# Kernel optimization log

Hardware: AMD Instinct MI355X
Metric: run time of the kernel (lower is better)

Reference implementation:

```python
import jax, jax.numpy as jnp
import numpy as np

B, S, H, D = 1, 2048, 16, 128
HID = H * D  # 2048
EPS = 1e-6


def setup_inputs() -> dict:
    key = jax.random.key(0)
    ks = jax.random.split(key, 6)
    sc = 1.0 / np.sqrt(HID)
    t = jnp.arange(S, dtype=jnp.float32)[:, None]
    inv = 1.0 / (10000.0 ** (jnp.arange(D // 2, dtype=jnp.float32) / (D // 2)))
    ang = t * inv[None, :]
    return {
        "hidden_states": jax.random.normal(ks[0], (B, S, HID), jnp.float32),
        "freqs_cos": jnp.cos(ang),
        "freqs_sin": jnp.sin(ang),
        "w_qkv": jax.random.normal(ks[1], (HID, 3 * HID), jnp.float32) * sc,
        "b_qkv": jnp.zeros((3 * HID,), jnp.float32),
        "w_norm_q": jnp.ones((HID,), jnp.float32),
        "w_norm_k": jnp.ones((HID,), jnp.float32),
        "w_out": jax.random.normal(ks[2], (HID, HID), jnp.float32) * sc,
        "b_out": jnp.zeros((HID,), jnp.float32),
    }


def _rmsnorm(x, w):
    var = jnp.mean(jnp.square(x), axis=-1, keepdims=True)
    return x * jax.lax.rsqrt(var + EPS) * w


def _rope(x, cos, sin):
    # x: [B, H, S, D]; cos/sin: [S, D//2], interleaved pair rotation
    xr = x.reshape(*x.shape[:-1], D // 2, 2)
    x1, x2 = xr[..., 0], xr[..., 1]
    c = cos[None, None, :, :]
    s = sin[None, None, :, :]
    o1 = x1 * c - x2 * s
    o2 = x1 * s + x2 * c
    return jnp.stack([o1, o2], axis=-1).reshape(x.shape)


def reference(hidden_states, freqs_cos, freqs_sin, w_qkv, b_qkv,
              w_norm_q, w_norm_k, w_out, b_out):
    qkv = hidden_states @ w_qkv + b_qkv  # [B, S, 3*HID]
    q, k, v = jnp.split(qkv, 3, axis=-1)
    q = _rmsnorm(q, w_norm_q).reshape(B, S, H, D).transpose(0, 2, 1, 3)
    k = _rmsnorm(k, w_norm_k).reshape(B, S, H, D).transpose(0, 2, 1, 3)
    v = v.reshape(B, S, H, D).transpose(0, 2, 1, 3)
    q = _rope(q, freqs_cos, freqs_sin)
    k = _rope(k, freqs_cos, freqs_sin)
    scale = 1.0 / np.sqrt(D)
    scores = jnp.einsum("bhqd,bhkd->bhqk", q, k) * scale
    attn = jax.nn.softmax(scores, axis=-1)
    out = jnp.einsum("bhqk,bhkd->bhqd", attn, v)
    out = out.transpose(0, 2, 1, 3).reshape(B, S, HID)
    return out @ w_out + b_out
```

## Files before the change

kernel.cpp:

```cpp
#include <hip/hip_runtime.h>
#include <math.h>

typedef unsigned short u16;
typedef __bf16 bf16x8 __attribute__((ext_vector_type(8)));
typedef float f32x4 __attribute__((ext_vector_type(4)));
typedef unsigned short u16x8 __attribute__((ext_vector_type(8)));

#define SLEN 2048
#define HIDN 2048
#define NH   16
#define DHD  128

static __device__ __forceinline__ float bf2f(u16 u) {
  unsigned int i = ((unsigned int)u) << 16;
  return __builtin_bit_cast(float, i);
}
static __device__ __forceinline__ u16 f2bf(float f) {
  unsigned int x = __builtin_bit_cast(unsigned int, f);
  unsigned int r = x + 0x7fffu + ((x >> 16) & 1u);
  return (u16)(r >> 16);
}
static __device__ __forceinline__ void gload_lds16(const u16* g, u16* l) {
  __builtin_amdgcn_global_load_lds((const __attribute__((address_space(1))) void*)g,
                                   (__attribute__((address_space(3))) void*)l,
                                   16, 0, 0);
}

__global__ __launch_bounds__(256) void transpcvt(const float* __restrict__ in,
                                                 u16* __restrict__ out,
                                                 int istride, int ostride) {
  __shared__ float tl[64][65];
  const int t = threadIdx.x;
  const int r0 = blockIdx.x * 64, c0 = blockIdx.y * 64;
#pragma unroll
  for (int it = 0; it < 4; ++it) {
    int row = it * 16 + (t >> 4);
    int col = (t & 15) * 4;
    f32x4 v = *(const f32x4*)&in[(size_t)(r0 + row) * istride + c0 + col];
    tl[row][col] = v[0]; tl[row][col + 1] = v[1];
    tl[row][col + 2] = v[2]; tl[row][col + 3] = v[3];
  }
  __syncthreads();
#pragma unroll
  for (int it = 0; it < 2; ++it) {
    int orow = it * 32 + (t >> 3);
    int ocol = (t & 7) * 8;
    u16x8 v;
#pragma unroll
    for (int j = 0; j < 8; ++j) v[j] = f2bf(tl[ocol + j][orow]);
    *(u16x8*)&out[(size_t)(c0 + orow) * ostride + r0 + ocol] = v;
  }
}

__global__ __launch_bounds__(256) void cvt_bf16(const float* __restrict__ in,
                                                u16* __restrict__ out) {
  int i = (blockIdx.x * 256 + threadIdx.x) * 8;
  f32x4 a = *(const f32x4*)&in[i];
  f32x4 b = *(const f32x4*)&in[i + 4];
  u16x8 v;
#pragma unroll
  for (int j = 0; j < 4; ++j) { v[j] = f2bf(a[j]); v[4 + j] = f2bf(b[j]); }
  *(u16x8*)&out[i] = v;
}

__global__ __launch_bounds__(256) void transp(const u16* __restrict__ in,
                                              u16* __restrict__ out,
                                              int istride, int ostride,
                                              int in_z, int out_z) {
  in  += (size_t)blockIdx.z * in_z;
  out += (size_t)blockIdx.z * out_z;
  __shared__ u16 tl[64][72];
  const int t  = threadIdx.x;
  const int r0 = blockIdx.x * 64, c0 = blockIdx.y * 64;
#pragma unroll
  for (int it = 0; it < 2; ++it) {
    int row = it * 32 + (t >> 3);
    int col = (t & 7) * 8;
    *(u16x8*)&tl[row][col] =
        *(const u16x8*)&in[(size_t)(r0 + row) * istride + c0 + col];
  }
  __syncthreads();
#pragma unroll
  for (int it = 0; it < 2; ++it) {
    int orow = it * 32 + (t >> 3);
    int ocol = (t & 7) * 8;
    u16x8 v;
#pragma unroll
    for (int j = 0; j < 8; ++j) v[j] = tl[ocol + j][orow];
    *(u16x8*)&out[(size_t)(c0 + orow) * ostride + r0 + ocol] = v;
  }
}

__global__ __launch_bounds__(256) void gemm_bt(const u16* __restrict__ A,
                                               const u16* __restrict__ BT,
                                               const float* __restrict__ bias,
                                               float* Cf, u16* Cb,
                                               int M, int N, int K) {
  __shared__ u16 lA[128 * 64];
  __shared__ u16 lB[128 * 64];
  const int t = threadIdx.x;
  const int lane = t & 63, w = t >> 6;
  const int g = lane >> 4, l16 = lane & 15;
  const int wr = w >> 1, wc = w & 1;
  const u16* Ab = A + (size_t)blockIdx.x * 128 * K;
  const u16* Bb = BT + (size_t)blockIdx.y * 128 * K;

  f32x4 acc[4][4];
#pragma unroll
  for (int mi = 0; mi < 4; ++mi)
#pragma unroll
    for (int ni = 0; ni < 4; ++ni) acc[mi][ni] = (f32x4)(0.0f);

  for (int k0 = 0; k0 < K; k0 += 64) {
    __syncthreads();
#pragma unroll
    for (int i = 0; i < 4; ++i) {
      int e = t * 8 + i * 2048;
      int row = e >> 6;
      int col16 = (e & 63) >> 3;
      int scol = (col16 ^ (row & 7)) * 8;
      gload_lds16(Ab + (size_t)row * K + k0 + scol, &lA[e]);
      gload_lds16(Bb + (size_t)row * K + k0 + scol, &lB[e]);
    }
    __syncthreads();
#pragma unroll
    for (int kk = 0; kk < 2; ++kk) {
      bf16x8 af[4], bfr[4];
#pragma unroll
      for (int mi = 0; mi < 4; ++mi) {
        int row = wr * 64 + mi * 16 + l16;
        af[mi] = *(const bf16x8*)&lA[row * 64 + (((4 * kk + g) ^ (l16 & 7)) << 3)];
      }
#pragma unroll
      for (int ni = 0; ni < 4; ++ni) {
        int row = wc * 64 + ni * 16 + l16;
        bfr[ni] = *(const bf16x8*)&lB[row * 64 + (((4 * kk + g) ^ (l16 & 7)) << 3)];
      }
#pragma unroll
      for (int mi = 0; mi < 4; ++mi)
#pragma unroll
        for (int ni = 0; ni < 4; ++ni)
          acc[mi][ni] = __builtin_amdgcn_mfma_f32_16x16x32_bf16(af[mi], bfr[ni],
                                                                acc[mi][ni], 0, 0, 0);
    }
  }

#pragma unroll
  for (int ni = 0; ni < 4; ++ni) {
    int n = blockIdx.y * 128 + wc * 64 + ni * 16 + l16;
    float bv = bias[n];
#pragma unroll
    for (int mi = 0; mi < 4; ++mi) {
      int m = blockIdx.x * 128 + wr * 64 + mi * 16 + 4 * g;
#pragma unroll
      for (int r = 0; r < 4; ++r) {
        float v = acc[mi][ni][r] + bv;
        if (Cf) Cf[(size_t)(m + r) * N + n] = v;
        else    Cb[(size_t)(m + r) * N + n] = f2bf(v);
      }
    }
  }
}

__global__ __launch_bounds__(256) void rms_rope(const u16* __restrict__ qkv,
                                                const float* __restrict__ fcos,
                                                const float* __restrict__ fsin,
                                                const float* __restrict__ wq,
                                                const float* __restrict__ wk,
                                                u16* __restrict__ Qr,
                                                u16* __restrict__ Kr) {
  const int s = blockIdx.x;
  const int t = threadIdx.x;
  const int lane = t & 63, w = t >> 6;
  __shared__ float red[2][4];
  const u16* row = qkv + (size_t)s * (3 * HIDN);

  u16x8 xq = *(const u16x8*)&row[t * 8];
  u16x8 xk = *(const u16x8*)&row[HIDN + t * 8];
  float fq[8], fk[8];
  float ssq = 0.f, ssk = 0.f;
#pragma unroll
  for (int j = 0; j < 8; ++j) {
    fq[j] = bf2f(xq[j]); ssq += fq[j] * fq[j];
    fk[j] = bf2f(xk[j]); ssk += fk[j] * fk[j];
  }
#pragma unroll
  for (int off = 32; off >= 1; off >>= 1) {
    ssq += __shfl_xor(ssq, off);
    ssk += __shfl_xor(ssk, off);
  }
  if (lane == 0) { red[0][w] = ssq; red[1][w] = ssk; }
  __syncthreads();
  float sq = red[0][0] + red[0][1] + red[0][2] + red[0][3];
  float sk = red[1][0] + red[1][1] + red[1][2] + red[1][3];
  float rq = rsqrtf(sq / (float)HIDN + 1e-6f);
  float rk = rsqrtf(sk / (float)HIDN + 1e-6f);

  f32x4 wq0 = *(const f32x4*)&wq[t * 8];
  f32x4 wq1 = *(const f32x4*)&wq[t * 8 + 4];
  f32x4 wk0 = *(const f32x4*)&wk[t * 8];
  f32x4 wk1 = *(const f32x4*)&wk[t * 8 + 4];
  float wqa[8] = {wq0[0], wq0[1], wq0[2], wq0[3], wq1[0], wq1[1], wq1[2], wq1[3]};
  float wka[8] = {wk0[0], wk0[1], wk0[2], wk0[3], wk1[0], wk1[1], wk1[2], wk1[3]};
  const int c0 = t * 8;
  const int h = c0 >> 7;
  const int d0 = c0 & 127;
  const int i0 = d0 >> 1;
  const float* cp = fcos + (size_t)s * (DHD / 2) + i0;
  const float* sp = fsin + (size_t)s * (DHD / 2) + i0;
  const float qscale = 0.12751744925f;

  u16x8 oq, ok;
#pragma unroll
  for (int p = 0; p < 4; ++p) {
    float c = cp[p], sn = sp[p];
    float q1 = fq[2 * p] * rq * wqa[2 * p];
    float q2 = fq[2 * p + 1] * rq * wqa[2 * p + 1];
    float k1 = fk[2 * p] * rk * wka[2 * p];
    float k2 = fk[2 * p + 1] * rk * wka[2 * p + 1];
    oq[2 * p]     = f2bf((q1 * c - q2 * sn) * qscale);
    oq[2 * p + 1] = f2bf((q1 * sn + q2 * c) * qscale);
    ok[2 * p]     = f2bf(k1 * c - k2 * sn);
    ok[2 * p + 1] = f2bf(k1 * sn + k2 * c);
  }
  size_t o = (size_t)h * SLEN * DHD + (size_t)s * DHD + d0;
  *(u16x8*)&Qr[o] = oq;
  *(u16x8*)&Kr[o] = ok;
}

__global__ __launch_bounds__(256) void attn_fwd(const u16* __restrict__ Qr,
                                                const u16* __restrict__ Kr,
                                                const u16* __restrict__ Vt,
                                                u16* __restrict__ out) {
  const int lin = blockIdx.x;
  const int xcd = lin & 7, idx = lin >> 3;
  const int h = xcd + ((idx >> 5) << 3);
  const int qb = idx & 31;
  const int t = threadIdx.x;
  const int lane = t & 63, w = t >> 6;
  const int g = lane >> 4, l16 = lane & 15;
  const int q0 = qb * 64 + w * 16;
  const u16* Qh = Qr + (size_t)h * SLEN * DHD;
  const u16* Kh = Kr + (size_t)h * SLEN * DHD;
  const u16* Vh = Vt + (size_t)h * DHD * SLEN;

  __shared__ u16 Kl[2][64 * 128];
  __shared__ u16 Vl[2][128 * 64];
  __shared__ u16 Pl[4][16][72];

  bf16x8 aq[4];
#pragma unroll
  for (int dk = 0; dk < 4; ++dk)
    aq[dk] = *(const bf16x8*)&Qh[(size_t)(q0 + l16) * DHD + dk * 32 + g * 8];

  f32x4 o[8];
#pragma unroll
  for (int df = 0; df < 8; ++df) o[df] = (f32x4)(0.0f);
  float m = -INFINITY, lsum = 0.f;

#pragma unroll
  for (int i = 0; i < 4; ++i) {
    int e = t * 8 + i * 2048;
    int kr = e >> 7, kc = (e & 127) >> 3;
    gload_lds16(Kh + (size_t)kr * DHD + ((kc ^ (kr & 7)) << 3), &Kl[0][e]);
    int vr = e >> 6, vc = (e & 63) >> 3;
    gload_lds16(Vh + (size_t)vr * SLEN + ((vc ^ (vr & 7)) << 3), &Vl[0][e]);
  }
  __syncthreads();

  int cur = 0;
  for (int kt = 0; kt < SLEN / 64; ++kt) {
    if (kt + 1 < SLEN / 64) {
      const int kv1 = (kt + 1) * 64;
#pragma unroll
      for (int i = 0; i < 4; ++i) {
        int e = t * 8 + i * 2048;
        int kr = e >> 7, kc = (e & 127) >> 3;
        gload_lds16(Kh + (size_t)(kv1 + kr) * DHD + ((kc ^ (kr & 7)) << 3),
                    &Kl[cur ^ 1][e]);
        int vr = e >> 6, vc = (e & 63) >> 3;
        gload_lds16(Vh + (size_t)vr * SLEN + kv1 + ((vc ^ (vr & 7)) << 3),
                    &Vl[cur ^ 1][e]);
      }
    }

    f32x4 s4[4];
#pragma unroll
    for (int nf = 0; nf < 4; ++nf) s4[nf] = (f32x4)(0.0f);
#pragma unroll
    for (int nf = 0; nf < 4; ++nf) {
#pragma unroll
      for (int dk = 0; dk < 4; ++dk) {
        bf16x8 bk = *(const bf16x8*)&Kl[cur][(nf * 16 + l16) * 128 +
                                            (((dk * 4 + g) ^ (l16 & 7)) << 3)];
        s4[nf] = __builtin_amdgcn_mfma_f32_16x16x32_bf16(bk, aq[dk], s4[nf], 0, 0, 0);
      }
    }
    float tm = s4[0][0];
#pragma unroll
    for (int nf = 0; nf < 4; ++nf)
#pragma unroll
      for (int r = 0; r < 4; ++r) tm = fmaxf(tm, s4[nf][r]);
    tm = fmaxf(tm, __shfl_xor(tm, 16));
    tm = fmaxf(tm, __shfl_xor(tm, 32));
    const bool nogrow = (tm <= m);
    const float mn = nogrow ? m : tm;
    float ls = 0.f;
#pragma unroll
    for (int nf = 0; nf < 4; ++nf)
#pragma unroll
      for (int r = 0; r < 4; ++r) {
        float p = exp2f(s4[nf][r] - mn);
        s4[nf][r] = p;
        ls += p;
      }
    ls += __shfl_xor(ls, 16);
    ls += __shfl_xor(ls, 32);
    if (__all(nogrow)) {
      lsum += ls;
    } else {
      float corr = exp2f(m - mn);
      m = mn;
      lsum = lsum * corr + ls;
#pragma unroll
      for (int r = 0; r < 4; ++r) {
        float cr = __shfl(corr, 20 * g + r);
#pragma unroll
        for (int df = 0; df < 8; ++df) o[df][r] *= cr;
      }
    }
#pragma unroll
    for (int nf = 0; nf < 4; ++nf)
#pragma unroll
      for (int r = 0; r < 4; ++r)
        Pl[w][l16][nf * 16 + 4 * g + r] = f2bf(s4[nf][r]);
#pragma unroll
    for (int ks = 0; ks < 2; ++ks) {
      bf16x8 ap = *(const bf16x8*)&Pl[w][l16][ks * 32 + g * 8];
#pragma unroll
      for (int df = 0; df < 8; ++df) {
        bf16x8 bv = *(const bf16x8*)&Vl[cur][(df * 16 + l16) * 64 +
                                             (((ks * 4 + g) ^ (l16 & 7)) << 3)];
        o[df] = __builtin_amdgcn_mfma_f32_16x16x32_bf16(ap, bv, o[df], 0, 0, 0);
      }
    }
    __syncthreads();
    cur ^= 1;
  }

  const float invq = 1.0f / lsum;
#pragma unroll
  for (int r = 0; r < 4; ++r) {
    float ir = __shfl(invq, 20 * g + r);
#pragma unroll
    for (int df = 0; df < 8; ++df)
      out[(size_t)(q0 + 4 * g + r) * HIDN + h * DHD + df * 16 + l16] =
          f2bf(o[df][r] * ir);
  }
}

extern "C" void kernel_launch(void* const* d_in, const int* in_sizes, int n_in,
                              void* d_out, int out_size, void* d_ws, size_t ws_size,
                              hipStream_t stream) {
  (void)in_sizes; (void)n_in; (void)out_size; (void)ws_size;
  const float* hs   = (const float*)d_in[0];
  const float* fc   = (const float*)d_in[1];
  const float* fs   = (const float*)d_in[2];
  const float* wqkv = (const float*)d_in[3];
  const float* bqkv = (const float*)d_in[4];
  const float* wnq  = (const float*)d_in[5];
  const float* wnk  = (const float*)d_in[6];
  const float* wout = (const float*)d_in[7];
  const float* bout = (const float*)d_in[8];
  float* out = (float*)d_out;
  char* ws = (char*)d_ws;

  u16* wqkvT = (u16*)(ws);
  u16* woutT = (u16*)(ws + 25165824);
  u16* qkv   = (u16*)(ws + 33554432);
  u16* hsB   = (u16*)(ws + 58720256);
  u16* Qr    = (u16*)(ws + 58720256);
  u16* Kr    = (u16*)(ws + 67108864);
  u16* Vt    = (u16*)(ws + 75497472);
  u16* attnO = (u16*)(ws + 83886080);

  transpcvt<<<dim3(32, 96), 256, 0, stream>>>(wqkv, wqkvT, 6144, 2048);
  transpcvt<<<dim3(32, 32), 256, 0, stream>>>(wout, woutT, 2048, 2048);
  cvt_bf16<<<dim3(2048), 256, 0, stream>>>(hs, hsB);
  gemm_bt<<<dim3(16, 48), 256, 0, stream>>>(hsB, wqkvT, bqkv, nullptr, qkv,
                                            2048, 6144, 2048);
  rms_rope<<<dim3(2048), 256, 0, stream>>>(qkv, fc, fs, wnq, wnk, Qr, Kr);
  transp<<<dim3(32, 2, 16), 256, 0, stream>>>(qkv + 4096, Vt, 6144, 2048, 128, 262144);
  attn_fwd<<<dim3(512), 256, 0, stream>>>(Qr, Kr, Vt, attnO);
  gemm_bt<<<dim3(16, 16), 256, 0, stream>>>(attnO, woutT, bout, out, nullptr,
                                            2048, 2048, 2048);
}
```

Baseline: 214.2 us.

## Remap GEMM blocks per XCD, read V directly from global, add setprio and occupancy hint

The GEMM moves to a 1D grid whose blocks are remapped so that each XCD handles a contiguous band of M rows. This is meant to improve L2 reuse of the A tiles. The attention kernel drops the V staging through LDS and reads V fragments straight from global memory, which frees LDS and allows a launch bound of three blocks per CU. It also raises wave priority around the MFMA sections. The cost is uncoalesced, latency-exposed global reads of V inside the inner loop, which the higher occupancy and L2 caching may or may not hide.

```diff
diff --git a/kernel.cpp b/kernel.cpp
--- a/kernel.cpp
+++ b/kernel.cpp
@@ -96,14 +96,21 @@
                                                const float* __restrict__ bias,
                                                float* Cf, u16* Cb,
                                                int M, int N, int K) {
+  const int nby = N >> 7;
+  const int lin = blockIdx.x;
+  const int xcd = lin & 7, idx = lin >> 3;
+  const int bpx = (M >> 7) >> 3;
+  const int bx = xcd * bpx + idx / nby;
+  const int by = idx % nby;
+
   __shared__ u16 lA[128 * 64];
   __shared__ u16 lB[128 * 64];
   const int t = threadIdx.x;
   const int lane = t & 63, w = t >> 6;
   const int g = lane >> 4, l16 = lane & 15;
   const int wr = w >> 1, wc = w & 1;
-  const u16* Ab = A + (size_t)blockIdx.x * 128 * K;
-  const u16* Bb = BT + (size_t)blockIdx.y * 128 * K;
+  const u16* Ab = A + (size_t)bx * 128 * K;
+  const u16* Bb = BT + (size_t)by * 128 * K;
 
   f32x4 acc[4][4];
 #pragma unroll
@@ -147,11 +154,11 @@
 
 #pragma unroll
   for (int ni = 0; ni < 4; ++ni) {
-    int n = blockIdx.y * 128 + wc * 64 + ni * 16 + l16;
+    int n = by * 128 + wc * 64 + ni * 16 + l16;
     float bv = bias[n];
 #pragma unroll
     for (int mi = 0; mi < 4; ++mi) {
-      int m = blockIdx.x * 128 + wr * 64 + mi * 16 + 4 * g;
+      int m = bx * 128 + wr * 64 + mi * 16 + 4 * g;
 #pragma unroll
       for (int r = 0; r < 4; ++r) {
         float v = acc[mi][ni][r] + bv;
@@ -228,10 +235,10 @@
   *(u16x8*)&Kr[o] = ok;
 }
 
-__global__ __launch_bounds__(256) void attn_fwd(const u16* __restrict__ Qr,
-                                                const u16* __restrict__ Kr,
-                                                const u16* __restrict__ Vt,
-                                                u16* __restrict__ out) {
+__global__ __launch_bounds__(256, 3) void attn_fwd(const u16* __restrict__ Qr,
+                                                   const u16* __restrict__ Kr,
+                                                   const u16* __restrict__ Vt,
+                                                   u16* __restrict__ out) {
   const int lin = blockIdx.x;
   const int xcd = lin & 7, idx = lin >> 3;
   const int h = xcd + ((idx >> 5) << 3);
@@ -245,7 +252,6 @@
   const u16* Vh = Vt + (size_t)h * DHD * SLEN;
 
   __shared__ u16 Kl[2][64 * 128];
-  __shared__ u16 Vl[2][128 * 64];
   __shared__ u16 Pl[4][16][72];
 
   bf16x8 aq[4];
@@ -263,30 +269,27 @@
     int e = t * 8 + i * 2048;
     int kr = e >> 7, kc = (e & 127) >> 3;
     gload_lds16(Kh + (size_t)kr * DHD + ((kc ^ (kr & 7)) << 3), &Kl[0][e]);
-    int vr = e >> 6, vc = (e & 63) >> 3;
-    gload_lds16(Vh + (size_t)vr * SLEN + ((vc ^ (vr & 7)) << 3), &Vl[0][e]);
   }
   __syncthreads();
 
   int cur = 0;
   for (int kt = 0; kt < SLEN / 64; ++kt) {
+    const int kv0 = kt * 64;
     if (kt + 1 < SLEN / 64) {
-      const int kv1 = (kt + 1) * 64;
+      const int kv1 = kv0 + 64;
 #pragma unroll
       for (int i = 0; i < 4; ++i) {
         int e = t * 8 + i * 2048;
         int kr = e >> 7, kc = (e & 127) >> 3;
         gload_lds16(Kh + (size_t)(kv1 + kr) * DHD + ((kc ^ (kr & 7)) << 3),
                     &Kl[cur ^ 1][e]);
-        int vr = e >> 6, vc = (e & 63) >> 3;
-        gload_lds16(Vh + (size_t)vr * SLEN + kv1 + ((vc ^ (vr & 7)) << 3),
-                    &Vl[cur ^ 1][e]);
       }
     }
 
     f32x4 s4[4];
 #pragma unroll
     for (int nf = 0; nf < 4; ++nf) s4[nf] = (f32x4)(0.0f);
+    __builtin_amdgcn_s_setprio(1);
 #pragma unroll
     for (int nf = 0; nf < 4; ++nf) {
 #pragma unroll
@@ -296,6 +299,7 @@
         s4[nf] = __builtin_amdgcn_mfma_f32_16x16x32_bf16(bk, aq[dk], s4[nf], 0, 0, 0);
       }
     }
+    __builtin_amdgcn_s_setprio(0);
     float tm = s4[0][0];
 #pragma unroll
     for (int nf = 0; nf < 4; ++nf)
@@ -337,12 +341,14 @@
 #pragma unroll
     for (int ks = 0; ks < 2; ++ks) {
       bf16x8 ap = *(const bf16x8*)&Pl[w][l16][ks * 32 + g * 8];
+      __builtin_amdgcn_s_setprio(1);
 #pragma unroll
       for (int df = 0; df < 8; ++df) {
-        bf16x8 bv = *(const bf16x8*)&Vl[cur][(df * 16 + l16) * 64 +
-                                             (((ks * 4 + g) ^ (l16 & 7)) << 3)];
+        bf16x8 bv = *(const bf16x8*)&Vh[(size_t)(df * 16 + l16) * SLEN +
+                                        kv0 + ks * 32 + g * 8];
         o[df] = __builtin_amdgcn_mfma_f32_16x16x32_bf16(ap, bv, o[df], 0, 0, 0);
       }
+      __builtin_amdgcn_s_setprio(0);
     }
     __syncthreads();
     cur ^= 1;
@@ -387,11 +393,11 @@
   transpcvt<<<dim3(32, 96), 256, 0, stream>>>(wqkv, wqkvT, 6144, 2048);
   transpcvt<<<dim3(32, 32), 256, 0, stream>>>(wout, woutT, 2048, 2048);
   cvt_bf16<<<dim3(2048), 256, 0, stream>>>(hs, hsB);
-  gemm_bt<<<dim3(16, 48), 256, 0, stream>>>(hsB, wqkvT, bqkv, nullptr, qkv,
-                                            2048, 6144, 2048);
+  gemm_bt<<<dim3(768), 256, 0, stream>>>(hsB, wqkvT, bqkv, nullptr, qkv,
+                                         2048, 6144, 2048);
   rms_rope<<<dim3(2048), 256, 0, stream>>>(qkv, fc, fs, wnq, wnk, Qr, Kr);
   transp<<<dim3(32, 2, 16), 256, 0, stream>>>(qkv + 4096, Vt, 6144, 2048, 128, 262144);
   attn_fwd<<<dim3(512), 256, 0, stream>>>(Qr, Kr, Vt, attnO);
-  gemm_bt<<<dim3(16, 16), 256, 0, stream>>>(attnO, woutT, bout, out, nullptr,
-                                            2048, 2048, 2048);
-}
+  gemm_bt<<<dim3(256), 256, 0, stream>>>(attnO, woutT, bout, out, nullptr,
+                                         2048, 2048, 2048);
+}
```

Measured after the change: 294.0 us. 1.37x slower.
